# Kernel tuning notes

Hardware: AMD Instinct MI355X
Metric: run time of the kernel (lower is better)

The kernel has to match this reference:

```python
import jax, jax.numpy as jnp
import numpy as np

N, L, E, H = 4, 4096, 1024, 1024


def setup_inputs() -> dict:
    key = jax.random.key(0)
    ks = jax.random.split(key, 7)
    s_in = 1.0 / np.sqrt(E)
    return {
        "X_embed": jax.random.normal(ks[0], (N, L, E), dtype=jnp.float32),
        "Wq": jax.random.normal(ks[1], (H, E), dtype=jnp.float32) * s_in,
        "bq": jnp.zeros((H,), dtype=jnp.float32),
        "Wk": jax.random.normal(ks[2], (H, E), dtype=jnp.float32) * s_in,
        "bk": jnp.zeros((H,), dtype=jnp.float32),
        "Wv": jax.random.normal(ks[3], (H, E), dtype=jnp.float32) * s_in,
        "bv": jnp.zeros((H,), dtype=jnp.float32),
    }


def reference(X_embed, Wq, bq, Wk, bk, Wv, bv):
    # Linear projections: (N, L, E) @ (E, H) + (H,) -> (N, L, H)
    Q = jnp.einsum('nle,he->nlh', X_embed, Wq) + bq
    K = jnp.einsum('nle,he->nlh', X_embed, Wk) + bk
    V = jnp.einsum('nle,he->nlh', X_embed, Wv) + bv
    # Scores (N, L, L); original scales by sqrt(Out.shape[2]) == sqrt(L)
    S = jnp.einsum('nah,nbh->nab', Q, K) / jnp.asarray(np.sqrt(float(L)), dtype=Q.dtype)
    # Original softmax is over dim=1 (the query axis 'a')
    A = jax.nn.softmax(S, axis=1)
    # 'nll,nlh->nlh': diagonal of A times V, elementwise over h
    diag = jnp.diagonal(A, axis1=1, axis2=2)  # (N, L)
    return diag[:, :, None] * V
```

## Files before the change

kernel.cpp:

```cpp
#include <hip/hip_runtime.h>
#include <hip/hip_bf16.h>
#include <stdint.h>

#define NB 4
#define LS 4096
#define ED 1024
#define HD 1024
#define MR (NB * LS)
#define SCALE_S (1.0f / 64.0f)

typedef __attribute__((ext_vector_type(8))) short bf16x8;
typedef __attribute__((ext_vector_type(8))) int   i32x8;
typedef __attribute__((ext_vector_type(4))) float f32x4;

__device__ __forceinline__ unsigned short f2bf(float f) {
    union { float f; uint32_t u; } x; x.f = f;
    uint32_t r = x.u + 0x7fffu + ((x.u >> 16) & 1u);
    return (unsigned short)(r >> 16);
}

__device__ __forceinline__ void load_lds16(const void* g, void* s) {
    __builtin_amdgcn_global_load_lds(
        (const __attribute__((address_space(1))) void*)g,
        (__attribute__((address_space(3))) void*)s, 16, 0, 0);
}

#define XCHUNKS (MR * ED / 4)
#define WCHUNKS (3 * ED * ED / 4)
__global__ void __launch_bounds__(256) cast_all_k(
    const float4* __restrict__ X, const float4* __restrict__ wq,
    const float4* __restrict__ wk, const float4* __restrict__ wv,
    ushort4* __restrict__ Xb, ushort4* __restrict__ Wall)
{
    const int i = blockIdx.x * 256 + threadIdx.x;
    if (i < XCHUNKS) {
        const float4 v = X[i];
        ushort4 o; o.x = f2bf(v.x); o.y = f2bf(v.y); o.z = f2bf(v.z); o.w = f2bf(v.w);
        Xb[i] = o;
    } else if (i < XCHUNKS + WCHUNKS) {
        const int j = i - XCHUNKS;
        const int s = j >> 18, jj = j & 0x3ffff;
        const float4 v = (s == 0 ? wq : s == 1 ? wk : wv)[jj];
        ushort4 o; o.x = f2bf(v.x); o.y = f2bf(v.y); o.z = f2bf(v.z); o.w = f2bf(v.w);
        Wall[j] = o;
    }
}


__device__ __forceinline__ void read_af(bf16x8 (&af)[4][2], const char* base,
                                        int arow, int sw7, int quad) {
#pragma unroll
    for (int mf = 0; mf < 4; mf++) {
        const char* r = base + (arow + mf * 16) * 128;
        af[mf][0] = *(const bf16x8*)(r + ((quad * 16) ^ sw7));
        af[mf][1] = *(const bf16x8*)(r + ((64 + quad * 16) ^ sw7));
    }
}
__device__ __forceinline__ void read_wf(bf16x8 (&wf)[4], const char* base,
                                        int wrow, int ks64, int sw7, int quad) {
#pragma unroll
    for (int nf = 0; nf < 4; nf++)
        wf[nf] = *(const bf16x8*)(base + (wrow + nf * 16) * 128 + ((ks64 + quad * 16) ^ sw7));
}
template<int KS>
__device__ __forceinline__ void mfma16(f32x4 (&acc)[4][4], const bf16x8 (&af)[4][2],
                                       const bf16x8 (&wf)[4]) {
#pragma unroll
    for (int mf = 0; mf < 4; mf++)
#pragma unroll
        for (int nf = 0; nf < 4; nf++)
            acc[mf][nf] = __builtin_amdgcn_mfma_f32_16x16x32_bf16(
                wf[nf], af[mf][KS], acc[mf][nf], 0, 0, 0);
}

#define QK_BAR() do { asm volatile("" ::: "memory"); \
    __builtin_amdgcn_s_barrier(); asm volatile("" ::: "memory"); } while (0)
#define PH_MID() do { QK_BAR(); \
    asm volatile("s_waitcnt lgkmcnt(0)" ::: "memory"); \
    __builtin_amdgcn_sched_barrier(0); \
    __builtin_amdgcn_s_setprio(1); } while (0)
#define PH_END() do { __builtin_amdgcn_s_setprio(0); QK_BAR(); } while (0)
#define PH_END_VM6() do { __builtin_amdgcn_s_setprio(0); \
    asm volatile("s_waitcnt vmcnt(6)" ::: "memory"); QK_BAR(); } while (0)
#define PH_END_VM0() do { __builtin_amdgcn_s_setprio(0); \
    asm volatile("s_waitcnt vmcnt(0)" ::: "memory"); QK_BAR(); } while (0)

__global__ void __launch_bounds__(512, 2)
gemm_qk_fused8(const unsigned short* __restrict__ A,
               const unsigned short* __restrict__ W,
               const float* __restrict__ bq, const float* __restrict__ bk,
               unsigned char* __restrict__ Qf8t, unsigned char* __restrict__ Kf8t,
               float* __restrict__ diag)
{
    extern __shared__ char lds[];
    const int t = threadIdx.x;
    const int w = t >> 6, lane = t & 63, quad = lane >> 4, l16 = lane & 15;
    const int wm = w >> 1, wn = w & 1;

    const int swz = (blockIdx.x & 7) * 64 + (blockIdx.x >> 3);
    const long blockM = (long)(swz >> 3) * 256;
    const int  blockN = (swz & 7) * 128;

    const long srow = (long)(w * 8 + (lane >> 3)) * 2048
                    + (long)(((lane & 7) ^ (lane >> 3)) << 4);
    const char* gA  = (const char*)A + blockM * 2048 + srow;
    const char* gAh = gA + 128 * 2048;
    const char* gWq = (const char*)W + (long)blockN * 2048 + srow;
    const char* gWk = gWq + (long)1024 * 2048;
    char* dst = lds + w * 1024;

#define ST(G, OFF, KB) do { \
    load_lds16((G) + (KB), dst + (OFF)); \
    load_lds16((G) + 131072 + (KB), dst + (OFF) + 8192); } while (0)

    const char* A0 = lds;          const char* A1 = lds + 65536;
    const char* Q0 = lds + 32768;  const char* Q1 = lds + 65536 + 32768;
    const char* K0 = lds + 49152;  const char* K1 = lds + 65536 + 49152;

    const int arow = wm * 64 + l16;
    const int wrow = wn * 64 + l16;
    const int sw7  = (l16 & 7) << 4;

    f32x4 aq[4][4] = {}; f32x4 ak[4][4] = {};
    bf16x8 aF[4][2], wF[4];

    ST(gA, 0, 0); ST(gAh, 16384, 0); ST(gWq, 32768, 0); ST(gWk, 49152, 0);
    ST(gA, 65536, 128); ST(gAh, 65536 + 16384, 128); ST(gWq, 65536 + 32768, 128);
    asm volatile("s_waitcnt vmcnt(6)" ::: "memory");
    QK_BAR();

#pragma unroll 1
    for (int i = 0; i < 7; ++i) {
        const long k1 = (2L * i + 1) * 128, k2 = (2L * i + 2) * 128, k3 = (2L * i + 3) * 128;
        read_af(aF, A0, arow, sw7, quad);
        read_wf(wF, Q0, wrow, 0, sw7, quad);
        ST(gWk, 65536 + 49152, k1);
        asm volatile("s_waitcnt lgkmcnt(8)" ::: "memory");
        PH_MID(); mfma16<0>(aq, aF, wF); PH_END();
        read_wf(wF, Q0, wrow, 64, sw7, quad);
        ST(gA, 0, k2);
        PH_MID(); mfma16<1>(aq, aF, wF); PH_END();
        read_wf(wF, K0, wrow, 0, sw7, quad);
        ST(gAh, 16384, k2);
        PH_MID(); mfma16<0>(ak, aF, wF); PH_END();
        read_wf(wF, K0, wrow, 64, sw7, quad);
        ST(gWq, 32768, k2);
        PH_MID(); mfma16<1>(ak, aF, wF); PH_END_VM6();
        read_af(aF, A1, arow, sw7, quad);
        read_wf(wF, Q1, wrow, 0, sw7, quad);
        ST(gWk, 49152, k2);
        asm volatile("s_waitcnt lgkmcnt(8)" ::: "memory");
        PH_MID(); mfma16<0>(aq, aF, wF); PH_END();
        read_wf(wF, Q1, wrow, 64, sw7, quad);
        ST(gA, 65536, k3);
        PH_MID(); mfma16<1>(aq, aF, wF); PH_END();
        read_wf(wF, K1, wrow, 0, sw7, quad);
        ST(gAh, 65536 + 16384, k3);
        PH_MID(); mfma16<0>(ak, aF, wF); PH_END();
        read_wf(wF, K1, wrow, 64, sw7, quad);
        ST(gWq, 65536 + 32768, k3);
        PH_MID(); mfma16<1>(ak, aF, wF); PH_END_VM6();
    }
    {
        read_af(aF, A0, arow, sw7, quad);
        read_wf(wF, Q0, wrow, 0, sw7, quad);
        ST(gWk, 65536 + 49152, 15L * 128);
        asm volatile("s_waitcnt lgkmcnt(8)" ::: "memory");
        PH_MID(); mfma16<0>(aq, aF, wF); PH_END();
        read_wf(wF, Q0, wrow, 64, sw7, quad);
        PH_MID(); mfma16<1>(aq, aF, wF); PH_END();
        read_wf(wF, K0, wrow, 0, sw7, quad);
        PH_MID(); mfma16<0>(ak, aF, wF); PH_END();
        read_wf(wF, K0, wrow, 64, sw7, quad);
        PH_MID(); mfma16<1>(ak, aF, wF); PH_END_VM0();
        read_af(aF, A1, arow, sw7, quad);
        read_wf(wF, Q1, wrow, 0, sw7, quad);
        PH_MID(); mfma16<0>(aq, aF, wF); PH_END();
        read_wf(wF, Q1, wrow, 64, sw7, quad);
        PH_MID(); mfma16<1>(aq, aF, wF); PH_END();
        read_wf(wF, K1, wrow, 0, sw7, quad);
        PH_MID(); mfma16<0>(ak, aF, wF); PH_END();
        read_wf(wF, K1, wrow, 64, sw7, quad);
        PH_MID(); mfma16<1>(ak, aF, wF); PH_END();
    }
#undef ST

    float dp[4] = {0.f, 0.f, 0.f, 0.f};
#pragma unroll
    for (int nf = 0; nf < 4; nf++) {
        const int col = blockN + wn * 64 + nf * 16 + quad * 4;
        const float4 q4 = *(const float4*)(bq + col);
        const float4 k4 = *(const float4*)(bk + col);
#pragma unroll
        for (int mf = 0; mf < 4; mf++) {
            const size_t row = (size_t)(blockM + wm * 64 + mf * 16 + l16);
            const float vq0 = aq[mf][nf][0] + q4.x, vq1 = aq[mf][nf][1] + q4.y;
            const float vq2 = aq[mf][nf][2] + q4.z, vq3 = aq[mf][nf][3] + q4.w;
            const float vk0 = ak[mf][nf][0] + k4.x, vk1 = ak[mf][nf][1] + k4.y;
            const float vk2 = ak[mf][nf][2] + k4.z, vk3 = ak[mf][nf][3] + k4.w;
            uint32_t uq = 0, uk = 0;
            uq = __builtin_amdgcn_cvt_pk_fp8_f32(vq0, vq1, uq, false);
            uq = __builtin_amdgcn_cvt_pk_fp8_f32(vq2, vq3, uq, true);
            uk = __builtin_amdgcn_cvt_pk_fp8_f32(vk0, vk1, uk, false);
            uk = __builtin_amdgcn_cvt_pk_fp8_f32(vk2, vk3, uk, true);
            const size_t f8 = (row >> 4) * 16384 + (size_t)(col >> 4) * 256
                            + (row & 15) * 16 + (col & 15);
            *(uint32_t*)(Qf8t + f8) = uq;
            *(uint32_t*)(Kf8t + f8) = uk;
            dp[mf] += vq0 * vk0 + vq1 * vk1 + vq2 * vk2 + vq3 * vk3;
        }
    }
#pragma unroll
    for (int mf = 0; mf < 4; mf++) {
        float d = dp[mf];
        d += __shfl_xor(d, 16);
        d += __shfl_xor(d, 32);
        if (quad == 0)
            atomicAdd(&diag[blockM + wm * 64 + mf * 16 + l16], d);
    }
}

__global__ void __launch_bounds__(256)
gemm_v(const unsigned short* __restrict__ A,
       const unsigned short* __restrict__ Wv,
       const float* __restrict__ bv, float* __restrict__ outV)
{
    __shared__ unsigned short As[128 * 32];
    __shared__ unsigned short Bs[128 * 32];

    const int t = threadIdx.x;
    const int wid = t >> 6, lane = t & 63, quad = lane >> 4, l16 = lane & 15;
    const int m0 = (wid >> 1) * 64, n0 = (wid & 1) * 64;
    const long blockM = (long)blockIdx.y * 128;
    const int blockN = blockIdx.x * 128;

    const char* a_g = (const char*)(A  + (blockM + (t >> 2)) * (size_t)ED + (size_t)((t & 3) * 8));
    const char* b_g = (const char*)(Wv + ((size_t)blockN + (t >> 2)) * ED + (size_t)((t & 3) * 8));
    const size_t half = (size_t)64 * ED * 2;

    char* a_s0 = (char*)As + wid * 1024;
    char* b_s0 = (char*)Bs + wid * 1024;

    f32x4 acc[4][4] = {};

    for (int kt = 0; kt < ED; kt += 32) {
        const int kb = kt * 2;
        load_lds16(a_g + kb,        a_s0);
        load_lds16(a_g + kb + half, a_s0 + 4096);
        load_lds16(b_g + kb,        b_s0);
        load_lds16(b_g + kb + half, b_s0 + 4096);
        __syncthreads();

        bf16x8 aF[4], bF[4];
        const char* AsB = (const char*)As;
        const char* BsB = (const char*)Bs;
#pragma unroll
        for (int mf = 0; mf < 4; mf++)
            aF[mf] = *(const bf16x8*)(AsB + ((m0 + mf * 16 + l16) * 32 + quad * 8) * 2);
#pragma unroll
        for (int nf = 0; nf < 4; nf++)
            bF[nf] = *(const bf16x8*)(BsB + ((n0 + nf * 16 + l16) * 32 + quad * 8) * 2);
#pragma unroll
        for (int mf = 0; mf < 4; mf++)
#pragma unroll
            for (int nf = 0; nf < 4; nf++)
                acc[mf][nf] = __builtin_amdgcn_mfma_f32_16x16x32_bf16(
                    bF[nf], aF[mf], acc[mf][nf], 0, 0, 0);
        __syncthreads();
    }

#pragma unroll
    for (int mf = 0; mf < 4; mf++) {
        const size_t row = (size_t)(blockM + m0 + mf * 16 + l16);
#pragma unroll
        for (int nf = 0; nf < 4; nf++) {
            const int col = blockN + n0 + nf * 16 + quad * 4;
            const float4 b4 = *(const float4*)(bv + col);
            float4 o;
            o.x = acc[mf][nf][0] + b4.x; o.y = acc[mf][nf][1] + b4.y;
            o.z = acc[mf][nf][2] + b4.z; o.w = acc[mf][nf][3] + b4.w;
            *(float4*)(outV + row * 1024 + col) = o;
        }
    }
}

__global__ void __launch_bounds__(256)
gemm_f8_denom(const unsigned char* __restrict__ Qt,
              const unsigned char* __restrict__ Kt,
              float* __restrict__ denom)
{
    __shared__ __align__(16) unsigned char As[16384];
    __shared__ __align__(16) unsigned char Bs[16384];

    const int t = threadIdx.x;
    const int wid = t >> 6, lane = t & 63, quad = lane >> 4, l16 = lane & 15;
    const int m0 = (wid >> 1) * 64, n0 = (wid & 1) * 64;
    const size_t zoff = (size_t)blockIdx.z * LS * (size_t)HD;
    const unsigned char* A = Qt + zoff;
    const unsigned char* B = Kt + zoff;
    float* dn = denom + (size_t)blockIdx.z * LS;
    const int blockM = blockIdx.y * 128;
    const int blockN = blockIdx.x * 128;

    size_t aoff[4], boff[4];
#pragma unroll
    for (int j = 0; j < 4; j++) {
        const int iw = wid * 4 + j;
        const size_t lo = (size_t)((iw & 1) * 4 + (lane >> 4)) * 256 + (size_t)(lane & 15) * 16;
        aoff[j] = ((size_t)(blockM >> 4) + (iw >> 1)) * 16384 + lo;
        boff[j] = ((size_t)(blockN >> 4) + (iw >> 1)) * 16384 + lo;
    }

    f32x4 acc[4][4] = {};

    for (int kt = 0; kt < 8; kt++) {
        const size_t ko = (size_t)kt * 2048;
#pragma unroll
        for (int j = 0; j < 4; j++) {
            load_lds16(A + aoff[j] + ko, (char*)As + (wid * 4 + j) * 1024);
            load_lds16(B + boff[j] + ko, (char*)Bs + (wid * 4 + j) * 1024);
        }
        __syncthreads();

        i32x8 aF[4], bF[4];
#pragma unroll
        for (int mf = 0; mf < 4; mf++) {
            const int base = (((m0 >> 4) + mf) * 2048) + quad * 512 + l16 * 16;
            const int4 lo = *(const int4*)(As + base);
            const int4 hi = *(const int4*)(As + base + 256);
            aF[mf][0] = lo.x; aF[mf][1] = lo.y; aF[mf][2] = lo.z; aF[mf][3] = lo.w;
            aF[mf][4] = hi.x; aF[mf][5] = hi.y; aF[mf][6] = hi.z; aF[mf][7] = hi.w;
        }
#pragma unroll
        for (int nf = 0; nf < 4; nf++) {
            const int base = (((n0 >> 4) + nf) * 2048) + quad * 512 + l16 * 16;
            const int4 lo = *(const int4*)(Bs + base);
            const int4 hi = *(const int4*)(Bs + base + 256);
            bF[nf][0] = lo.x; bF[nf][1] = lo.y; bF[nf][2] = lo.z; bF[nf][3] = lo.w;
            bF[nf][4] = hi.x; bF[nf][5] = hi.y; bF[nf][6] = hi.z; bF[nf][7] = hi.w;
        }
#pragma unroll
        for (int mf = 0; mf < 4; mf++)
#pragma unroll
            for (int nf = 0; nf < 4; nf++)
                acc[mf][nf] = __builtin_amdgcn_mfma_scale_f32_16x16x128_f8f6f4(
                    aF[mf], bF[nf], acc[mf][nf],
                    0, 0,
                    0, 0x7f7f7f7f,
                    0, 0x7f7f7f7f);
        __syncthreads();
    }

#pragma unroll
    for (int nf = 0; nf < 4; nf++) {
        float s = 0.f;
#pragma unroll
        for (int mf = 0; mf < 4; mf++)
#pragma unroll
            for (int r = 0; r < 4; r++)
                s += __expf(acc[mf][nf][r] * SCALE_S);
        s += __shfl_xor(s, 16);
        s += __shfl_xor(s, 32);
        if (quad == 0)
            atomicAdd(&dn[blockN + n0 + nf * 16 + l16], s);
    }
}

__global__ void __launch_bounds__(256) finalize_k(
    float* __restrict__ out, const float* __restrict__ diag,
    const float* __restrict__ denom)
{
    const int row = blockIdx.x;
    const float sc = __expf(diag[row] * SCALE_S) / denom[row];
    float4* p = (float4*)(out + (size_t)row * HD) + threadIdx.x;
    float4 v = *p;
    v.x *= sc; v.y *= sc; v.z *= sc; v.w *= sc;
    *p = v;
}

extern "C" void kernel_launch(void* const* d_in, const int* in_sizes, int n_in,
                              void* d_out, int out_size, void* d_ws, size_t ws_size,
                              hipStream_t stream)
{
    (void)in_sizes; (void)n_in; (void)out_size; (void)ws_size;
    const float* X  = (const float*)d_in[0];
    const float* Wq = (const float*)d_in[1];
    const float* bq = (const float*)d_in[2];
    const float* Wk = (const float*)d_in[3];
    const float* bk = (const float*)d_in[4];
    const float* Wv = (const float*)d_in[5];
    const float* bv = (const float*)d_in[6];
    float* out = (float*)d_out;

    char* p = (char*)d_ws;
    unsigned short* Xb   = (unsigned short*)p; p += (size_t)MR * ED * 2;
    unsigned short* Wall = (unsigned short*)p; p += (size_t)3072 * ED * 2;
    unsigned char*  Qf8t = (unsigned char*)p;  p += (size_t)MR * HD;
    unsigned char*  Kf8t = (unsigned char*)p;  p += (size_t)MR * HD;
    float* diag  = (float*)p; p += (size_t)MR * 4;
    float* denom = (float*)p; p += (size_t)MR * 4;

    dim3 blk(256);

    static int qk8_init = 0;
    if (!qk8_init) {
        hipFuncSetAttribute((const void*)gemm_qk_fused8,
                            hipFuncAttributeMaxDynamicSharedMemorySize, 131072);
        qk8_init = 1;
    }

    cast_all_k<<<(XCHUNKS + WCHUNKS + 255) / 256, blk, 0, stream>>>(
        (const float4*)X, (const float4*)Wq, (const float4*)Wk, (const float4*)Wv,
        (ushort4*)Xb, (ushort4*)Wall);

    hipMemsetAsync(diag, 0, 2 * MR * sizeof(float), stream);

    gemm_qk_fused8<<<dim3(512), dim3(512), 131072, stream>>>(
        Xb, Wall, bq, bk, Qf8t, Kf8t, diag);

    dim3 gv(HD / 128, MR / 128);
    gemm_v<<<gv, blk, 0, stream>>>(Xb, Wall + (size_t)2048 * ED, bv, out);

    dim3 gden(LS / 128, LS / 128, NB);
    gemm_f8_denom<<<gden, blk, 0, stream>>>(Qf8t, Kf8t, denom);

    finalize_k<<<MR, blk, 0, stream>>>(out, diag, denom);
}
```

Baseline: 355.8 us.

## Rewrite fp8 denominator GEMM with 256x256 tiles and double-buffered LDS pipeline

Replaces the 128x128, single-buffered fp8 QK^T denominator kernel with a 512-thread, 256x256-tile kernel. It double-buffers global-to-LDS loads, interleaves them with MFMA phases under barriers and setprio, and swizzles block order so neighbouring blocks share tiles. The aim is to hide global load latency, raise arithmetic intensity per block, and cut the number of atomic adds per denominator element. In exchange it uses 128KB of dynamic LDS and more accumulator registers, which limits occupancy, and it depends on hand-tuned waitcnt values being correct.

Result: slower. 395.4 us (+11.1%).

```diff
diff --git a/kernel.cpp b/kernel.cpp
--- a/kernel.cpp
+++ b/kernel.cpp
@@ -46,33 +46,6 @@
     }
 }
 
-
-__device__ __forceinline__ void read_af(bf16x8 (&af)[4][2], const char* base,
-                                        int arow, int sw7, int quad) {
-#pragma unroll
-    for (int mf = 0; mf < 4; mf++) {
-        const char* r = base + (arow + mf * 16) * 128;
-        af[mf][0] = *(const bf16x8*)(r + ((quad * 16) ^ sw7));
-        af[mf][1] = *(const bf16x8*)(r + ((64 + quad * 16) ^ sw7));
-    }
-}
-__device__ __forceinline__ void read_wf(bf16x8 (&wf)[4], const char* base,
-                                        int wrow, int ks64, int sw7, int quad) {
-#pragma unroll
-    for (int nf = 0; nf < 4; nf++)
-        wf[nf] = *(const bf16x8*)(base + (wrow + nf * 16) * 128 + ((ks64 + quad * 16) ^ sw7));
-}
-template<int KS>
-__device__ __forceinline__ void mfma16(f32x4 (&acc)[4][4], const bf16x8 (&af)[4][2],
-                                       const bf16x8 (&wf)[4]) {
-#pragma unroll
-    for (int mf = 0; mf < 4; mf++)
-#pragma unroll
-        for (int nf = 0; nf < 4; nf++)
-            acc[mf][nf] = __builtin_amdgcn_mfma_f32_16x16x32_bf16(
-                wf[nf], af[mf][KS], acc[mf][nf], 0, 0, 0);
-}
-
 #define QK_BAR() do { asm volatile("" ::: "memory"); \
     __builtin_amdgcn_s_barrier(); asm volatile("" ::: "memory"); } while (0)
 #define PH_MID() do { QK_BAR(); \
@@ -84,6 +57,32 @@
     asm volatile("s_waitcnt vmcnt(6)" ::: "memory"); QK_BAR(); } while (0)
 #define PH_END_VM0() do { __builtin_amdgcn_s_setprio(0); \
     asm volatile("s_waitcnt vmcnt(0)" ::: "memory"); QK_BAR(); } while (0)
+
+__device__ __forceinline__ void read_af(bf16x8 (&af)[4][2], const char* base,
+                                        int arow, int sw7, int quad) {
+#pragma unroll
+    for (int mf = 0; mf < 4; mf++) {
+        const char* r = base + (arow + mf * 16) * 128;
+        af[mf][0] = *(const bf16x8*)(r + ((quad * 16) ^ sw7));
+        af[mf][1] = *(const bf16x8*)(r + ((64 + quad * 16) ^ sw7));
+    }
+}
+__device__ __forceinline__ void read_wf(bf16x8 (&wf)[4], const char* base,
+                                        int wrow, int ks64, int sw7, int quad) {
+#pragma unroll
+    for (int nf = 0; nf < 4; nf++)
+        wf[nf] = *(const bf16x8*)(base + (wrow + nf * 16) * 128 + ((ks64 + quad * 16) ^ sw7));
+}
+template<int KS>
+__device__ __forceinline__ void mfma16(f32x4 (&acc)[4][4], const bf16x8 (&af)[4][2],
+                                       const bf16x8 (&wf)[4]) {
+#pragma unroll
+    for (int mf = 0; mf < 4; mf++)
+#pragma unroll
+        for (int nf = 0; nf < 4; nf++)
+            acc[mf][nf] = __builtin_amdgcn_mfma_f32_16x16x32_bf16(
+                wf[nf], af[mf][KS], acc[mf][nf], 0, 0, 0);
+}
 
 __global__ void __launch_bounds__(512, 2)
 gemm_qk_fused8(const unsigned short* __restrict__ A,
@@ -284,85 +283,143 @@
     }
 }
 
-__global__ void __launch_bounds__(256)
-gemm_f8_denom(const unsigned char* __restrict__ Qt,
-              const unsigned char* __restrict__ Kt,
-              float* __restrict__ denom)
-{
-    __shared__ __align__(16) unsigned char As[16384];
-    __shared__ __align__(16) unsigned char Bs[16384];
-
+__device__ __forceinline__ void read_f8(i32x8 &f, const char* p) {
+    const int4 lo = *(const int4*)p;
+    const int4 hi = *(const int4*)(p + 256);
+    f[0] = lo.x; f[1] = lo.y; f[2] = lo.z; f[3] = lo.w;
+    f[4] = hi.x; f[5] = hi.y; f[6] = hi.z; f[7] = hi.w;
+}
+template<int MF0>
+__device__ __forceinline__ void dmfma8(f32x4 (&acc)[8][4], const i32x8 (&aF)[2],
+                                       const i32x8 (&bF)[4]) {
+#pragma unroll
+    for (int j = 0; j < 2; j++)
+#pragma unroll
+        for (int nf = 0; nf < 4; nf++)
+            acc[MF0 + j][nf] = __builtin_amdgcn_mfma_scale_f32_16x16x128_f8f6f4(
+                aF[j], bF[nf], acc[MF0 + j][nf],
+                0, 0, 0, 0x7f7f7f7f, 0, 0x7f7f7f7f);
+}
+
+__global__ void __launch_bounds__(512, 2)
+gemm_f8_denom8(const unsigned char* __restrict__ Qt,
+               const unsigned char* __restrict__ Kt,
+               float* __restrict__ denom)
+{
+    extern __shared__ char lds[];
     const int t = threadIdx.x;
-    const int wid = t >> 6, lane = t & 63, quad = lane >> 4, l16 = lane & 15;
-    const int m0 = (wid >> 1) * 64, n0 = (wid & 1) * 64;
-    const size_t zoff = (size_t)blockIdx.z * LS * (size_t)HD;
-    const unsigned char* A = Qt + zoff;
-    const unsigned char* B = Kt + zoff;
-    float* dn = denom + (size_t)blockIdx.z * LS;
-    const int blockM = blockIdx.y * 128;
-    const int blockN = blockIdx.x * 128;
-
-    size_t aoff[4], boff[4];
-#pragma unroll
-    for (int j = 0; j < 4; j++) {
-        const int iw = wid * 4 + j;
-        const size_t lo = (size_t)((iw & 1) * 4 + (lane >> 4)) * 256 + (size_t)(lane & 15) * 16;
-        aoff[j] = ((size_t)(blockM >> 4) + (iw >> 1)) * 16384 + lo;
-        boff[j] = ((size_t)(blockN >> 4) + (iw >> 1)) * 16384 + lo;
-    }
-
-    f32x4 acc[4][4] = {};
-
-    for (int kt = 0; kt < 8; kt++) {
-        const size_t ko = (size_t)kt * 2048;
-#pragma unroll
-        for (int j = 0; j < 4; j++) {
-            load_lds16(A + aoff[j] + ko, (char*)As + (wid * 4 + j) * 1024);
-            load_lds16(B + boff[j] + ko, (char*)Bs + (wid * 4 + j) * 1024);
-        }
-        __syncthreads();
-
-        i32x8 aF[4], bF[4];
-#pragma unroll
-        for (int mf = 0; mf < 4; mf++) {
-            const int base = (((m0 >> 4) + mf) * 2048) + quad * 512 + l16 * 16;
-            const int4 lo = *(const int4*)(As + base);
-            const int4 hi = *(const int4*)(As + base + 256);
-            aF[mf][0] = lo.x; aF[mf][1] = lo.y; aF[mf][2] = lo.z; aF[mf][3] = lo.w;
-            aF[mf][4] = hi.x; aF[mf][5] = hi.y; aF[mf][6] = hi.z; aF[mf][7] = hi.w;
-        }
-#pragma unroll
-        for (int nf = 0; nf < 4; nf++) {
-            const int base = (((n0 >> 4) + nf) * 2048) + quad * 512 + l16 * 16;
-            const int4 lo = *(const int4*)(Bs + base);
-            const int4 hi = *(const int4*)(Bs + base + 256);
-            bF[nf][0] = lo.x; bF[nf][1] = lo.y; bF[nf][2] = lo.z; bF[nf][3] = lo.w;
-            bF[nf][4] = hi.x; bF[nf][5] = hi.y; bF[nf][6] = hi.z; bF[nf][7] = hi.w;
-        }
-#pragma unroll
-        for (int mf = 0; mf < 4; mf++)
-#pragma unroll
-            for (int nf = 0; nf < 4; nf++)
-                acc[mf][nf] = __builtin_amdgcn_mfma_scale_f32_16x16x128_f8f6f4(
-                    aF[mf], bF[nf], acc[mf][nf],
-                    0, 0,
-                    0, 0x7f7f7f7f,
-                    0, 0x7f7f7f7f);
-        __syncthreads();
-    }
-
+    const int w = t >> 6, lane = t & 63, quad = lane >> 4, l16 = lane & 15;
+    const int wm = w >> 2, wn = w & 3;
+
+    const int pos = (blockIdx.x & 7) * 128 + (blockIdx.x >> 3);
+    const int z = pos >> 8;
+    const int rem = pos & 255;
+    const int blockM = (rem >> 4) * 256;
+    const int blockN = (rem & 15) * 256;
+
+    const size_t zoff = (size_t)z * LS * (size_t)HD;
+    const long stg = (long)(t >> 7) * 16384 + (long)(t & 127) * 16;
+    const unsigned char* gA = Qt + zoff + (size_t)(blockM >> 4) * 16384 + stg;
+    const unsigned char* gB = Kt + zoff + (size_t)(blockN >> 4) * 16384 + stg;
+
+    char* const A0 = lds;
+    char* const B0 = lds + 32768;
+    char* const A1 = lds + 65536;
+    char* const B1 = lds + 98304;
+
+#define STA_(REG, J, KT) load_lds16(gA + (long)(J) * 65536 + (long)(KT) * 2048, \
+                                    (REG) + (J) * 8192 + w * 1024)
+#define STB_(REG, J, KT) load_lds16(gB + (long)(J) * 65536 + (long)(KT) * 2048, \
+                                    (REG) + (J) * 8192 + w * 1024)
+
+    const int abase = (wm * 8) * 2048 + quad * 512 + l16 * 16;
+    const int bbase = (wn * 4) * 2048 + quad * 512 + l16 * 16;
+
+    f32x4 acc[8][4] = {};
+    i32x8 aF[2], bF[4];
+
+    STA_(A0, 0, 0); STA_(A0, 1, 0); STA_(A0, 2, 0); STA_(A0, 3, 0);
+    STB_(B0, 0, 0); STB_(B0, 1, 0); STB_(B0, 2, 0); STB_(B0, 3, 0);
+    STB_(B1, 0, 1); STB_(B1, 1, 1); STB_(B1, 2, 1); STB_(B1, 3, 1);
+    STA_(A1, 0, 1); STA_(A1, 2, 1);
+    asm volatile("s_waitcnt vmcnt(6)" ::: "memory");
+    QK_BAR();
+
+#pragma unroll 1
+    for (int i = 0; i < 3; ++i) {
+        const int k1 = 2 * i + 1, k2 = 2 * i + 2, k3 = 2 * i + 3;
+        read_f8(bF[0], B0 + bbase);        read_f8(bF[1], B0 + bbase + 2048);
+        read_f8(bF[2], B0 + bbase + 4096); read_f8(bF[3], B0 + bbase + 6144);
+        read_f8(aF[0], A0 + abase);        read_f8(aF[1], A0 + abase + 2048);
+        STA_(A1, 1, k1); STA_(A1, 3, k1);
+        asm volatile("s_waitcnt lgkmcnt(8)" ::: "memory");
+        PH_MID(); dmfma8<0>(acc, aF, bF); PH_END();
+        read_f8(aF[0], A0 + abase + 4096); read_f8(aF[1], A0 + abase + 6144);
+        STB_(B0, 0, k2); STB_(B0, 1, k2);
+        PH_MID(); dmfma8<2>(acc, aF, bF); PH_END();
+        read_f8(aF[0], A0 + abase + 8192); read_f8(aF[1], A0 + abase + 10240);
+        STB_(B0, 2, k2); STB_(B0, 3, k2);
+        PH_MID(); dmfma8<4>(acc, aF, bF); PH_END();
+        read_f8(aF[0], A0 + abase + 12288); read_f8(aF[1], A0 + abase + 14336);
+        STA_(A0, 0, k2); STA_(A0, 2, k2);
+        PH_MID(); dmfma8<6>(acc, aF, bF); PH_END_VM6();
+        read_f8(bF[0], B1 + bbase);        read_f8(bF[1], B1 + bbase + 2048);
+        read_f8(bF[2], B1 + bbase + 4096); read_f8(bF[3], B1 + bbase + 6144);
+        read_f8(aF[0], A1 + abase);        read_f8(aF[1], A1 + abase + 2048);
+        STA_(A0, 1, k2); STA_(A0, 3, k2);
+        asm volatile("s_waitcnt lgkmcnt(8)" ::: "memory");
+        PH_MID(); dmfma8<0>(acc, aF, bF); PH_END();
+        read_f8(aF[0], A1 + abase + 4096); read_f8(aF[1], A1 + abase + 6144);
+        STB_(B1, 0, k3); STB_(B1, 1, k3);
+        PH_MID(); dmfma8<2>(acc, aF, bF); PH_END();
+        read_f8(aF[0], A1 + abase + 8192); read_f8(aF[1], A1 + abase + 10240);
+        STB_(B1, 2, k3); STB_(B1, 3, k3);
+        PH_MID(); dmfma8<4>(acc, aF, bF); PH_END();
+        read_f8(aF[0], A1 + abase + 12288); read_f8(aF[1], A1 + abase + 14336);
+        STA_(A1, 0, k3); STA_(A1, 2, k3);
+        PH_MID(); dmfma8<6>(acc, aF, bF); PH_END_VM6();
+    }
+    {
+        read_f8(bF[0], B0 + bbase);        read_f8(bF[1], B0 + bbase + 2048);
+        read_f8(bF[2], B0 + bbase + 4096); read_f8(bF[3], B0 + bbase + 6144);
+        read_f8(aF[0], A0 + abase);        read_f8(aF[1], A0 + abase + 2048);
+        STA_(A1, 1, 7); STA_(A1, 3, 7);
+        asm volatile("s_waitcnt lgkmcnt(8)" ::: "memory");
+        PH_MID(); dmfma8<0>(acc, aF, bF); PH_END();
+        read_f8(aF[0], A0 + abase + 4096); read_f8(aF[1], A0 + abase + 6144);
+        PH_MID(); dmfma8<2>(acc, aF, bF); PH_END();
+        read_f8(aF[0], A0 + abase + 8192); read_f8(aF[1], A0 + abase + 10240);
+        PH_MID(); dmfma8<4>(acc, aF, bF); PH_END();
+        read_f8(aF[0], A0 + abase + 12288); read_f8(aF[1], A0 + abase + 14336);
+        PH_MID(); dmfma8<6>(acc, aF, bF); PH_END_VM0();
+        read_f8(bF[0], B1 + bbase);        read_f8(bF[1], B1 + bbase + 2048);
+        read_f8(bF[2], B1 + bbase + 4096); read_f8(bF[3], B1 + bbase + 6144);
+        read_f8(aF[0], A1 + abase);        read_f8(aF[1], A1 + abase + 2048);
+        PH_MID(); dmfma8<0>(acc, aF, bF); PH_END();
+        read_f8(aF[0], A1 + abase + 4096); read_f8(aF[1], A1 + abase + 6144);
+        PH_MID(); dmfma8<2>(acc, aF, bF); PH_END();
+        read_f8(aF[0], A1 + abase + 8192); read_f8(aF[1], A1 + abase + 10240);
+        PH_MID(); dmfma8<4>(acc, aF, bF); PH_END();
+        read_f8(aF[0], A1 + abase + 12288); read_f8(aF[1], A1 + abase + 14336);
+        PH_MID(); dmfma8<6>(acc, aF, bF);
+        __builtin_amdgcn_s_setprio(0);
+    }
+#undef STA_
+#undef STB_
+
+    float* dn = denom + (size_t)z * LS;
 #pragma unroll
     for (int nf = 0; nf < 4; nf++) {
         float s = 0.f;
 #pragma unroll
-        for (int mf = 0; mf < 4; mf++)
+        for (int mf = 0; mf < 8; mf++)
 #pragma unroll
             for (int r = 0; r < 4; r++)
                 s += __expf(acc[mf][nf][r] * SCALE_S);
         s += __shfl_xor(s, 16);
         s += __shfl_xor(s, 32);
         if (quad == 0)
-            atomicAdd(&dn[blockN + n0 + nf * 16 + l16], s);
+            atomicAdd(&dn[blockN + wn * 64 + nf * 16 + l16], s);
     }
 }
 
@@ -402,11 +459,13 @@
 
     dim3 blk(256);
 
-    static int qk8_init = 0;
-    if (!qk8_init) {
+    static int init8 = 0;
+    if (!init8) {
         hipFuncSetAttribute((const void*)gemm_qk_fused8,
                             hipFuncAttributeMaxDynamicSharedMemorySize, 131072);
-        qk8_init = 1;
+        hipFuncSetAttribute((const void*)gemm_f8_denom8,
+                            hipFuncAttributeMaxDynamicSharedMemorySize, 131072);
+        init8 = 1;
     }
 
     cast_all_k<<<(XCHUNKS + WCHUNKS + 255) / 256, blk, 0, stream>>>(
@@ -421,8 +480,7 @@
     dim3 gv(HD / 128, MR / 128);
     gemm_v<<<gv, blk, 0, stream>>>(Xb, Wall + (size_t)2048 * ED, bv, out);
 
-    dim3 gden(LS / 128, LS / 128, NB);
-    gemm_f8_denom<<<gden, blk, 0, stream>>>(Qf8t, Kf8t, denom);
+    gemm_f8_denom8<<<dim3(1024), dim3(512), 131072, stream>>>(Qf8t, Kf8t, denom);
 
     finalize_k<<<MR, blk, 0, stream>>>(out, diag, denom);
 }
```

## Fuse V projection with softmax-diagonal scaling in pipelined 256x128 GEMM

Applied to the files above, without the earlier changes.

Replaces the simple single-buffered V GEMM and the separate finalize pass with one kernel. The new kernel uses 512-thread blocks with 256x128 tiles, a triple-buffered LDS pipeline built on direct global-to-LDS loads with swizzling, and an epilogue that applies the bias and the exp(diag)/denom scale before writing the output. This removes one full read-modify-write pass over the 64 MB fp32 output and raises MFMA throughput in the V GEMM. The V GEMM now runs after the denominator kernel, so it can no longer overlap with it. The launch-bounds attribute on the QK kernel is also rewritten as waves_per_eu.

Result: faster. 313.5 us (median of 2 runs) (-11.9%).

```diff
diff --git a/kernel.cpp b/kernel.cpp
--- a/kernel.cpp
+++ b/kernel.cpp
@@ -46,33 +46,6 @@
     }
 }
 
-
-__device__ __forceinline__ void read_af(bf16x8 (&af)[4][2], const char* base,
-                                        int arow, int sw7, int quad) {
-#pragma unroll
-    for (int mf = 0; mf < 4; mf++) {
-        const char* r = base + (arow + mf * 16) * 128;
-        af[mf][0] = *(const bf16x8*)(r + ((quad * 16) ^ sw7));
-        af[mf][1] = *(const bf16x8*)(r + ((64 + quad * 16) ^ sw7));
-    }
-}
-__device__ __forceinline__ void read_wf(bf16x8 (&wf)[4], const char* base,
-                                        int wrow, int ks64, int sw7, int quad) {
-#pragma unroll
-    for (int nf = 0; nf < 4; nf++)
-        wf[nf] = *(const bf16x8*)(base + (wrow + nf * 16) * 128 + ((ks64 + quad * 16) ^ sw7));
-}
-template<int KS>
-__device__ __forceinline__ void mfma16(f32x4 (&acc)[4][4], const bf16x8 (&af)[4][2],
-                                       const bf16x8 (&wf)[4]) {
-#pragma unroll
-    for (int mf = 0; mf < 4; mf++)
-#pragma unroll
-        for (int nf = 0; nf < 4; nf++)
-            acc[mf][nf] = __builtin_amdgcn_mfma_f32_16x16x32_bf16(
-                wf[nf], af[mf][KS], acc[mf][nf], 0, 0, 0);
-}
-
 #define QK_BAR() do { asm volatile("" ::: "memory"); \
     __builtin_amdgcn_s_barrier(); asm volatile("" ::: "memory"); } while (0)
 #define PH_MID() do { QK_BAR(); \
@@ -85,7 +58,33 @@
 #define PH_END_VM0() do { __builtin_amdgcn_s_setprio(0); \
     asm volatile("s_waitcnt vmcnt(0)" ::: "memory"); QK_BAR(); } while (0)
 
-__global__ void __launch_bounds__(512, 2)
+__device__ __forceinline__ void read_af(bf16x8 (&af)[4][2], const char* base,
+                                        int arow, int sw7, int quad) {
+#pragma unroll
+    for (int mf = 0; mf < 4; mf++) {
+        const char* r = base + (arow + mf * 16) * 128;
+        af[mf][0] = *(const bf16x8*)(r + ((quad * 16) ^ sw7));
+        af[mf][1] = *(const bf16x8*)(r + ((64 + quad * 16) ^ sw7));
+    }
+}
+__device__ __forceinline__ void read_wf(bf16x8 (&wf)[4], const char* base,
+                                        int wrow, int ks64, int sw7, int quad) {
+#pragma unroll
+    for (int nf = 0; nf < 4; nf++)
+        wf[nf] = *(const bf16x8*)(base + (wrow + nf * 16) * 128 + ((ks64 + quad * 16) ^ sw7));
+}
+template<int KS>
+__device__ __forceinline__ void mfma16(f32x4 (&acc)[4][4], const bf16x8 (&af)[4][2],
+                                       const bf16x8 (&wf)[4]) {
+#pragma unroll
+    for (int mf = 0; mf < 4; mf++)
+#pragma unroll
+        for (int nf = 0; nf < 4; nf++)
+            acc[mf][nf] = __builtin_amdgcn_mfma_f32_16x16x32_bf16(
+                wf[nf], af[mf][KS], acc[mf][nf], 0, 0, 0);
+}
+
+__global__ void __launch_bounds__(512) __attribute__((amdgpu_waves_per_eu(2, 2)))
 gemm_qk_fused8(const unsigned short* __restrict__ A,
                const unsigned short* __restrict__ W,
                const float* __restrict__ bq, const float* __restrict__ bk,
@@ -221,70 +220,6 @@
 }
 
 __global__ void __launch_bounds__(256)
-gemm_v(const unsigned short* __restrict__ A,
-       const unsigned short* __restrict__ Wv,
-       const float* __restrict__ bv, float* __restrict__ outV)
-{
-    __shared__ unsigned short As[128 * 32];
-    __shared__ unsigned short Bs[128 * 32];
-
-    const int t = threadIdx.x;
-    const int wid = t >> 6, lane = t & 63, quad = lane >> 4, l16 = lane & 15;
-    const int m0 = (wid >> 1) * 64, n0 = (wid & 1) * 64;
-    const long blockM = (long)blockIdx.y * 128;
-    const int blockN = blockIdx.x * 128;
-
-    const char* a_g = (const char*)(A  + (blockM + (t >> 2)) * (size_t)ED + (size_t)((t & 3) * 8));
-    const char* b_g = (const char*)(Wv + ((size_t)blockN + (t >> 2)) * ED + (size_t)((t & 3) * 8));
-    const size_t half = (size_t)64 * ED * 2;
-
-    char* a_s0 = (char*)As + wid * 1024;
-    char* b_s0 = (char*)Bs + wid * 1024;
-
-    f32x4 acc[4][4] = {};
-
-    for (int kt = 0; kt < ED; kt += 32) {
-        const int kb = kt * 2;
-        load_lds16(a_g + kb,        a_s0);
-        load_lds16(a_g + kb + half, a_s0 + 4096);
-        load_lds16(b_g + kb,        b_s0);
-        load_lds16(b_g + kb + half, b_s0 + 4096);
-        __syncthreads();
-
-        bf16x8 aF[4], bF[4];
-        const char* AsB = (const char*)As;
-        const char* BsB = (const char*)Bs;
-#pragma unroll
-        for (int mf = 0; mf < 4; mf++)
-            aF[mf] = *(const bf16x8*)(AsB + ((m0 + mf * 16 + l16) * 32 + quad * 8) * 2);
-#pragma unroll
-        for (int nf = 0; nf < 4; nf++)
-            bF[nf] = *(const bf16x8*)(BsB + ((n0 + nf * 16 + l16) * 32 + quad * 8) * 2);
-#pragma unroll
-        for (int mf = 0; mf < 4; mf++)
-#pragma unroll
-            for (int nf = 0; nf < 4; nf++)
-                acc[mf][nf] = __builtin_amdgcn_mfma_f32_16x16x32_bf16(
-                    bF[nf], aF[mf], acc[mf][nf], 0, 0, 0);
-        __syncthreads();
-    }
-
-#pragma unroll
-    for (int mf = 0; mf < 4; mf++) {
-        const size_t row = (size_t)(blockM + m0 + mf * 16 + l16);
-#pragma unroll
-        for (int nf = 0; nf < 4; nf++) {
-            const int col = blockN + n0 + nf * 16 + quad * 4;
-            const float4 b4 = *(const float4*)(bv + col);
-            float4 o;
-            o.x = acc[mf][nf][0] + b4.x; o.y = acc[mf][nf][1] + b4.y;
-            o.z = acc[mf][nf][2] + b4.z; o.w = acc[mf][nf][3] + b4.w;
-            *(float4*)(outV + row * 1024 + col) = o;
-        }
-    }
-}
-
-__global__ void __launch_bounds__(256)
 gemm_f8_denom(const unsigned char* __restrict__ Qt,
               const unsigned char* __restrict__ Kt,
               float* __restrict__ denom)
@@ -366,16 +301,91 @@
     }
 }
 
-__global__ void __launch_bounds__(256) finalize_k(
-    float* __restrict__ out, const float* __restrict__ diag,
-    const float* __restrict__ denom)
+__global__ void __launch_bounds__(512)
+gemm_v8fin(const unsigned short* __restrict__ A,
+           const unsigned short* __restrict__ Wv,
+           const float* __restrict__ bv, const float* __restrict__ diag,
+           const float* __restrict__ denom, float* __restrict__ out)
 {
-    const int row = blockIdx.x;
-    const float sc = __expf(diag[row] * SCALE_S) / denom[row];
-    float4* p = (float4*)(out + (size_t)row * HD) + threadIdx.x;
-    float4 v = *p;
-    v.x *= sc; v.y *= sc; v.z *= sc; v.w *= sc;
-    *p = v;
+    extern __shared__ char lds[];
+    const int t = threadIdx.x;
+    const int w = t >> 6, lane = t & 63, quad = lane >> 4, l16 = lane & 15;
+    const int wm = w >> 1, wn = w & 1;
+
+    const int swz = (blockIdx.x & 7) * 64 + (blockIdx.x >> 3);
+    const long blockM = (long)(swz >> 3) * 256;
+    const int  blockN = (swz & 7) * 128;
+
+    const int scol = (((t & 3) ^ ((t >> 2) & 3)) << 4);
+    const char* gA0 = (const char*)A + (blockM + (t >> 2)) * 2048 + scol;
+    const char* gA1 = gA0 + 128 * 2048;
+    const char* gW0 = (const char*)Wv + ((long)blockN + (t >> 2)) * 2048 + scol;
+
+    const int arow = wm * 64 + l16;
+    const int wrow = wn * 64 + l16;
+    const int rdoff = (quad * 16) ^ ((l16 & 3) << 4);
+
+    f32x4 acc[4][4] = {};
+    bf16x8 aF[4], wF[4];
+
+#define VBA(J) (lds + (J) * 24576)
+#define VST(J, KT) do { \
+    load_lds16(gA0 + (long)(KT) * 64, VBA(J) + w * 1024); \
+    load_lds16(gA1 + (long)(KT) * 64, VBA(J) + 8192 + w * 1024); \
+    load_lds16(gW0 + (long)(KT) * 64, VBA(J) + 16384 + w * 1024); } while (0)
+#define VREAD(J) do { \
+    const char* Ab_ = VBA(J); const char* Wb_ = VBA(J) + 16384; \
+    _Pragma("unroll") for (int mf = 0; mf < 4; mf++) \
+        aF[mf] = *(const bf16x8*)(Ab_ + (arow + mf * 16) * 64 + rdoff); \
+    _Pragma("unroll") for (int nf = 0; nf < 4; nf++) \
+        wF[nf] = *(const bf16x8*)(Wb_ + (wrow + nf * 16) * 64 + rdoff); } while (0)
+#define VCOMP() do { \
+    asm volatile("s_waitcnt lgkmcnt(0)" ::: "memory"); \
+    __builtin_amdgcn_sched_barrier(0); \
+    __builtin_amdgcn_s_setprio(1); \
+    _Pragma("unroll") for (int mf = 0; mf < 4; mf++) \
+    _Pragma("unroll") for (int nf = 0; nf < 4; nf++) \
+        acc[mf][nf] = __builtin_amdgcn_mfma_f32_16x16x32_bf16( \
+            wF[nf], aF[mf], acc[mf][nf], 0, 0, 0); \
+    __builtin_amdgcn_s_setprio(0); } while (0)
+#define VEND3() do { asm volatile("s_waitcnt vmcnt(3)" ::: "memory"); QK_BAR(); } while (0)
+
+    VST(0, 0); VST(1, 1);
+    asm volatile("s_waitcnt vmcnt(3)" ::: "memory");
+    QK_BAR();
+
+#pragma unroll 1
+    for (int i = 0; i < 10; ++i) {
+        const int b = 3 * i;
+        VREAD(0); VST(2, b + 2); VCOMP(); VEND3();
+        VREAD(1); VST(0, b + 3); VCOMP(); VEND3();
+        VREAD(2); VST(1, b + 4); VCOMP(); VEND3();
+    }
+    VREAD(0); VCOMP();
+    asm volatile("s_waitcnt vmcnt(0)" ::: "memory"); QK_BAR();
+    VREAD(1); VCOMP();
+#undef VBA
+#undef VST
+#undef VREAD
+#undef VCOMP
+#undef VEND3
+
+#pragma unroll
+    for (int mf = 0; mf < 4; mf++) {
+        const long row = blockM + wm * 64 + mf * 16 + l16;
+        const float sc = __expf(diag[row] * SCALE_S) / denom[row];
+#pragma unroll
+        for (int nf = 0; nf < 4; nf++) {
+            const int col = blockN + wn * 64 + nf * 16 + quad * 4;
+            const float4 b4 = *(const float4*)(bv + col);
+            float4 o;
+            o.x = (acc[mf][nf][0] + b4.x) * sc;
+            o.y = (acc[mf][nf][1] + b4.y) * sc;
+            o.z = (acc[mf][nf][2] + b4.z) * sc;
+            o.w = (acc[mf][nf][3] + b4.w) * sc;
+            *(float4*)(out + row * 1024 + col) = o;
+        }
+    }
 }
 
 extern "C" void kernel_launch(void* const* d_in, const int* in_sizes, int n_in,
@@ -402,11 +412,13 @@
 
     dim3 blk(256);
 
-    static int qk8_init = 0;
-    if (!qk8_init) {
+    static int init8 = 0;
+    if (!init8) {
         hipFuncSetAttribute((const void*)gemm_qk_fused8,
                             hipFuncAttributeMaxDynamicSharedMemorySize, 131072);
-        qk8_init = 1;
+        hipFuncSetAttribute((const void*)gemm_v8fin,
+                            hipFuncAttributeMaxDynamicSharedMemorySize, 73728);
+        init8 = 1;
     }
 
     cast_all_k<<<(XCHUNKS + WCHUNKS + 255) / 256, blk, 0, stream>>>(
@@ -418,11 +430,9 @@
     gemm_qk_fused8<<<dim3(512), dim3(512), 131072, stream>>>(
         Xb, Wall, bq, bk, Qf8t, Kf8t, diag);
 
-    dim3 gv(HD / 128, MR / 128);
-    gemm_v<<<gv, blk, 0, stream>>>(Xb, Wall + (size_t)2048 * ED, bv, out);
-
     dim3 gden(LS / 128, LS / 128, NB);
     gemm_f8_denom<<<gden, blk, 0, stream>>>(Qf8t, Kf8t, denom);
 
-    finalize_k<<<MR, blk, 0, stream>>>(out, diag, denom);
-}
+    gemm_v8fin<<<dim3(512), dim3(512), 73728, stream>>>(
+        Xb, Wall + (size_t)2048 * ED, bv, diag, denom, out);
+}
```
